# Performance work log

Hardware: AMD Instinct MI355X
Metric: run time of the kernel (lower is better)

## Reference

```python
import jax, jax.numpy as jnp
import numpy as np

B, S, E, H = 2, 2048, 1024, 16
D = E // H  # head_dim = 64
NEG = -1e9


def setup_inputs() -> dict:
    key = jax.random.key(0)
    ks = jax.random.split(key, 12)
    def xavier(k, shape):
        fan_in, fan_out = shape[1], shape[0]
        lim = jnp.sqrt(6.0 / (fan_in + fan_out))
        return jax.random.uniform(k, shape, jnp.float32, -lim, lim)
    inp = {
        'Q_input': jax.random.normal(ks[0], (B, S, E), jnp.float32),
        'K_input': jax.random.normal(ks[1], (B, S, E), jnp.float32),
        'V_input': jax.random.normal(ks[2], (B, S, E), jnp.float32),
        'causal_mask': jnp.where(jnp.tril(jnp.ones((S, S), bool)), 0.0, NEG).astype(jnp.float32),
        'padding_mask': jnp.zeros((B, S), bool),
        'W_q': xavier(ks[3], (E, E)), 'b_q': jnp.zeros((E,), jnp.float32),
        'W_k': xavier(ks[4], (E, E)), 'b_k': jnp.zeros((E,), jnp.float32),
        'W_v': xavier(ks[5], (E, E)), 'b_v': jnp.zeros((E,), jnp.float32),
        'W_o': xavier(ks[6], (E, E)), 'b_o': jnp.zeros((E,), jnp.float32),
    }
    return inp


def reference(Q_input, K_input, V_input, causal_mask, padding_mask,
              W_q, b_q, W_k, b_k, W_v, b_v, W_o, b_o):
    b = Q_input.shape[0]
    # linear proj (torch convention: x @ W.T + b), split into heads -> [B,H,S,D]
    def proj(x, W, bias):
        y = x @ W.T + bias
        return y.reshape(b, -1, H, D).transpose(0, 2, 1, 3)
    Q = proj(Q_input, W_q, b_q)
    K = proj(K_input, W_k, b_k)
    V = proj(V_input, W_v, b_v)
    scale = 1.0 / jnp.sqrt(jnp.float32(D))
    scores = jnp.einsum('bhqd,bhkd->bhqk', Q, K) * scale  # [B,H,Sq,Sk]
    scores = jnp.where(padding_mask[:, None, None, :], NEG, scores)
    scores = scores + causal_mask  # broadcasts [Sq,Sk]
    attn = jax.nn.softmax(scores, axis=-1)
    ctx = jnp.einsum('bhqk,bhkd->bhqd', attn, V)
    ctx = ctx.transpose(0, 2, 1, 3).reshape(b, -1, E)
    return ctx @ W_o.T + b_o
```

## Files before the change

kernel.cpp:

```cpp
#include <hip/hip_runtime.h>
#include <hip/hip_bf16.h>

#define B_ 2
#define S_ 2048
#define E_ 1024
#define H_ 16
#define D_ 64

typedef __bf16 bf16x8 __attribute__((ext_vector_type(8)));
typedef __bf16 bf16x4 __attribute__((ext_vector_type(4)));
typedef float f32x4 __attribute__((ext_vector_type(4)));

#define MFMA16(a, b, c) __builtin_amdgcn_mfma_f32_16x16x32_bf16(a, b, c, 0, 0, 0)

__device__ __forceinline__ void cp16(const void* g, void* l) {
  __builtin_amdgcn_global_load_lds((const __attribute__((address_space(1))) void*)g,
                                   (__attribute__((address_space(3))) void*)l, 16, 0, 0);
}

__global__ __launch_bounds__(256) void cast_all(
    const float* __restrict__ w0, const float* __restrict__ w1,
    const float* __restrict__ w2, const float* __restrict__ w3,
    const float* __restrict__ x0, const float* __restrict__ x1,
    const float* __restrict__ x2,
    __bf16* __restrict__ dW, __bf16* __restrict__ dX)
{
  const int id = blockIdx.x;
  const float* src;
  __bf16* dst;
  size_t i;
  if (id < 2048) {
    const float* ws[4] = {w0, w1, w2, w3};
    int w = id >> 9;
    src = ws[w];
    dst = dW + (size_t)w * E_ * E_;
    i = ((size_t)(id & 511) * 256 + threadIdx.x) * 8;
  } else {
    int e = id - 2048;
    const float* xs[3] = {x0, x1, x2};
    int x = e >> 11;
    src = xs[x];
    dst = dX + (size_t)x * B_ * S_ * E_;
    i = ((size_t)(e & 2047) * 256 + threadIdx.x) * 8;
  }
  f32x4 a = *(const f32x4*)(src + i);
  f32x4 b = *(const f32x4*)(src + i + 4);
  bf16x8 o;
#pragma unroll
  for (int j = 0; j < 4; ++j) { o[j] = (__bf16)a[j]; o[j + 4] = (__bf16)b[j]; }
  *(bf16x8*)(dst + i) = o;
}

__global__ __launch_bounds__(256) void gemm_qkv(
    const __bf16* __restrict__ Xb, const __bf16* __restrict__ Wc,
    const float* __restrict__ bq, const float* __restrict__ bk,
    const float* __restrict__ bv, __bf16* __restrict__ Proj,
    __bf16* __restrict__ Vt)
{
  __shared__ __bf16 As[2][128 * 32];
  __shared__ __bf16 Bs[2][128 * 32];

  const int tid  = threadIdx.x;
  const int wave = tid >> 6, lane = tid & 63;
  const int l15  = lane & 15, quad = lane >> 4;
  const int wr = wave >> 1, wc = wave & 1;
  const int m0 = blockIdx.x * 128;
  const int wid = blockIdx.y >> 3;
  const int n0 = (blockIdx.y & 7) * 128;

  const __bf16* X   = Xb + (size_t)wid * B_ * S_ * E_;
  const float* bias = wid == 0 ? bq : (wid == 1 ? bk : bv);
  const __bf16* W   = Wc + (size_t)wid * E_ * E_;
  __bf16* Out       = Proj + (size_t)wid * B_ * S_ * E_;

  auto stage = [&](int k0, int bi) {
#pragma unroll
    for (int i = 0; i < 2; ++i) {
      int c = i * 256 + tid;
      int row = c >> 2, cg = c & 3;
      cp16(X + (size_t)(m0 + row) * E_ + k0 + cg * 8,
           (char*)&As[bi][0] + i * 4096 + wave * 1024);
    }
#pragma unroll
    for (int i = 0; i < 2; ++i) {
      int c = i * 256 + tid;
      int row = c >> 2, cg = c & 3;
      cp16(W + (size_t)(n0 + row) * E_ + k0 + cg * 8,
           (char*)&Bs[bi][0] + i * 4096 + wave * 1024);
    }
  };

  f32x4 acc[4][4];
#pragma unroll
  for (int i = 0; i < 4; ++i)
#pragma unroll
    for (int j = 0; j < 4; ++j) acc[i][j] = (f32x4){0, 0, 0, 0};

  stage(0, 0);
  int cur = 0;
  for (int k0 = 0; k0 < E_; k0 += 32) {
    if (k0 + 32 < E_) {
      stage(k0 + 32, cur ^ 1);
      asm volatile("s_waitcnt vmcnt(4)" ::: "memory");
    } else {
      asm volatile("s_waitcnt vmcnt(0)" ::: "memory");
    }
    __builtin_amdgcn_s_barrier();

    bf16x8 af[4], bfr[4];
#pragma unroll
    for (int ms = 0; ms < 4; ++ms) {
      int row = wr * 64 + ms * 16 + l15;
      af[ms] = *(const bf16x8*)((const char*)&As[cur][0] + row * 64 + quad * 16);
    }
#pragma unroll
    for (int ns = 0; ns < 4; ++ns) {
      int row = wc * 64 + ns * 16 + l15;
      bfr[ns] = *(const bf16x8*)((const char*)&Bs[cur][0] + row * 64 + quad * 16);
    }
    __builtin_amdgcn_s_setprio(1);
#pragma unroll
    for (int ms = 0; ms < 4; ++ms)
#pragma unroll
      for (int ns = 0; ns < 4; ++ns)
        acc[ms][ns] = MFMA16(af[ms], bfr[ns], acc[ms][ns]);
    __builtin_amdgcn_s_setprio(0);

    asm volatile("" ::: "memory");
    __builtin_amdgcn_s_barrier();
    asm volatile("" ::: "memory");
    cur ^= 1;
  }

  if (wid == 2) {
#pragma unroll
    for (int ns = 0; ns < 4; ++ns) {
      int n = n0 + wc * 64 + ns * 16 + l15;
      float bv_ = bias[n];
      int m_base = m0 + wr * 64 + quad * 4;
      int b = m_base >> 11;
      int s_base = m_base & 2047;
      __bf16* vdst = Vt + (size_t)(b * H_ * D_ + n) * S_ + s_base;
#pragma unroll
      for (int ms = 0; ms < 4; ++ms)
#pragma unroll
        for (int r = 0; r < 4; ++r)
          vdst[ms * 16 + r] = (__bf16)(acc[ms][ns][r] + bv_);
    }
  } else {
    const float osc = (wid == 0) ? 0.18033688011f : 1.0f;
#pragma unroll
    for (int ns = 0; ns < 4; ++ns) {
      int n = n0 + wc * 64 + ns * 16 + l15;
      float bv_ = bias[n];
#pragma unroll
      for (int ms = 0; ms < 4; ++ms)
#pragma unroll
        for (int r = 0; r < 4; ++r) {
          int m = m0 + wr * 64 + ms * 16 + quad * 4 + r;
          Out[(size_t)m * E_ + n] = (__bf16)((acc[ms][ns][r] + bv_) * osc);
        }
    }
  }
}

__global__ __launch_bounds__(256) void gemm_out(
    const __bf16* __restrict__ X, const __bf16* __restrict__ W,
    const float* __restrict__ bias, float* __restrict__ out)
{
  __shared__ __bf16 As[2][64 * 32];
  __shared__ __bf16 Bs[2][128 * 32];

  const int tid  = threadIdx.x;
  const int wave = tid >> 6, lane = tid & 63;
  const int l15  = lane & 15, quad = lane >> 4;
  const int wr = wave >> 1, wc = wave & 1;
  const int m0 = blockIdx.x * 64;
  const int n0 = blockIdx.y * 128;

  auto stage = [&](int k0, int bi) {
    {
      int row = tid >> 2, cg = tid & 3;
      cp16(X + (size_t)(m0 + row) * E_ + k0 + cg * 8,
           (char*)&As[bi][0] + wave * 1024);
    }
#pragma unroll
    for (int i = 0; i < 2; ++i) {
      int c = i * 256 + tid;
      int row = c >> 2, cg = c & 3;
      cp16(W + (size_t)(n0 + row) * E_ + k0 + cg * 8,
           (char*)&Bs[bi][0] + i * 4096 + wave * 1024);
    }
  };

  f32x4 acc[2][4];
#pragma unroll
  for (int i = 0; i < 2; ++i)
#pragma unroll
    for (int j = 0; j < 4; ++j) acc[i][j] = (f32x4){0, 0, 0, 0};

  stage(0, 0);
  int cur = 0;
  for (int k0 = 0; k0 < E_; k0 += 32) {
    if (k0 + 32 < E_) {
      stage(k0 + 32, cur ^ 1);
      asm volatile("s_waitcnt vmcnt(3)" ::: "memory");
    } else {
      asm volatile("s_waitcnt vmcnt(0)" ::: "memory");
    }
    __builtin_amdgcn_s_barrier();

    bf16x8 af[2], bfr[4];
#pragma unroll
    for (int ms = 0; ms < 2; ++ms) {
      int row = wr * 32 + ms * 16 + l15;
      af[ms] = *(const bf16x8*)((const char*)&As[cur][0] + row * 64 + quad * 16);
    }
#pragma unroll
    for (int ns = 0; ns < 4; ++ns) {
      int row = wc * 64 + ns * 16 + l15;
      bfr[ns] = *(const bf16x8*)((const char*)&Bs[cur][0] + row * 64 + quad * 16);
    }
    __builtin_amdgcn_s_setprio(1);
#pragma unroll
    for (int ms = 0; ms < 2; ++ms)
#pragma unroll
      for (int ns = 0; ns < 4; ++ns)
        acc[ms][ns] = MFMA16(af[ms], bfr[ns], acc[ms][ns]);
    __builtin_amdgcn_s_setprio(0);

    asm volatile("" ::: "memory");
    __builtin_amdgcn_s_barrier();
    asm volatile("" ::: "memory");
    cur ^= 1;
  }

#pragma unroll
  for (int ns = 0; ns < 4; ++ns) {
    int n = n0 + wc * 64 + ns * 16 + l15;
    float bv_ = bias[n];
#pragma unroll
    for (int ms = 0; ms < 2; ++ms)
#pragma unroll
      for (int r = 0; r < 4; ++r) {
        int m = m0 + wr * 32 + ms * 16 + quad * 4 + r;
        out[(size_t)m * E_ + n] = acc[ms][ns][r] + bv_;
      }
  }
}

__global__ __launch_bounds__(128, 4) void attn_fwd(
    const __bf16* __restrict__ Qp, const __bf16* __restrict__ Kp,
    const __bf16* __restrict__ Vt, __bf16* __restrict__ Ctx)
{
  const int tid  = threadIdx.x;
  const int wave = tid >> 6;
  const int lane = tid & 63;
  const int l15  = lane & 15;
  const int quad = lane >> 4;
  const int id   = blockIdx.x;
  const int bh   = (id & 7) * 4 + ((id >> 3) & 3);
  const int tile = 63 - (id >> 5);
  const int b    = bh >> 4;
  const int h    = bh & 15;
  const int wq0  = tile * 32 + wave * 16;

  __shared__ __bf16 Ksh[64 * 64];
  __shared__ __bf16 Vsh[64 * 64];

  const __bf16* Khb = Kp + (size_t)b * S_ * E_ + h * 64;
  const __bf16* Vhb = Vt + ((size_t)b * H_ + h) * D_ * S_;

  bf16x8 qa[2];
#pragma unroll
  for (int kk = 0; kk < 2; ++kk)
    qa[kk] = *(const bf16x8*)&Qp[(size_t)(b * S_ + wq0 + l15) * E_ +
                                 h * 64 + kk * 32 + quad * 8];

  f32x4 o[4];
  float rs = 0.f;
#pragma unroll
  for (int ds = 0; ds < 4; ++ds) o[ds] = (f32x4){0, 0, 0, 0};

  const int nch = (tile >> 1) + 1;

  uint4 gk[4], gv[4];
  const int ccr = tid >> 3;
  const int ccg = tid & 7;

  auto issue = [&](int c) {
    const int kb0 = c * 64;
#pragma unroll
    for (int i = 0; i < 4; ++i) {
      int key = i * 16 + ccr;
      const void* ga = Khb + (size_t)(kb0 + key) * E_ + ccg * 8;
      asm volatile("global_load_dwordx4 %0, %1, off"
                   : "=v"(gk[i]) : "v"(ga) : "memory");
    }
#pragma unroll
    for (int i = 0; i < 4; ++i) {
      int d = i * 16 + ccr;
      const void* ga = Vhb + (size_t)d * S_ + kb0 + ccg * 8;
      asm volatile("global_load_dwordx4 %0, %1, off"
                   : "=v"(gv[i]) : "v"(ga) : "memory");
    }
  };
  auto commit = [&]() {
#pragma unroll
    for (int i = 0; i < 4; ++i) {
      int key = i * 16 + ccr;
      *(uint4*)((char*)Ksh + key * 128 + ((ccg ^ (key & 7)) * 16)) = gk[i];
    }
#pragma unroll
    for (int i = 0; i < 4; ++i) {
      int d = i * 16 + ccr;
      *(uint4*)((char*)Vsh + d * 128 + ((ccg ^ (d & 7)) * 16)) = gv[i];
    }
  };

  issue(0);
  asm volatile("s_waitcnt vmcnt(0)" ::: "memory");
  __builtin_amdgcn_sched_barrier(0);
  commit();
  asm volatile("s_waitcnt lgkmcnt(0)" ::: "memory");
  asm volatile("" ::: "memory");
  __builtin_amdgcn_s_barrier();

  for (int c = 0; c < nch; ++c) {
    if (c + 1 < nch) issue(c + 1);
    const int kb0 = c * 64;

    f32x4 sc[4];
    __builtin_amdgcn_s_setprio(1);
#pragma unroll
    for (int ks = 0; ks < 4; ++ks) {
      int row = ks * 16 + l15;
      bf16x8 kf0 = *(const bf16x8*)((const char*)Ksh + row * 128 + (((quad)     ^ (l15 & 7)) * 16));
      bf16x8 kf1 = *(const bf16x8*)((const char*)Ksh + row * 128 + (((4 + quad) ^ (l15 & 7)) * 16));
      f32x4 s = {0, 0, 0, 0};
      s = MFMA16(kf0, qa[0], s);
      s = MFMA16(kf1, qa[1], s);
      sc[ks] = s;
    }
    __builtin_amdgcn_s_setprio(0);

    unsigned pw[4][2];
    const bool msk = (kb0 + 63 > wq0);
    if (msk) {
#pragma unroll
      for (int ks = 0; ks < 4; ++ks) {
        float p[4];
#pragma unroll
        for (int r = 0; r < 4; ++r) {
          float e = exp2f(sc[ks][r]);
          if (kb0 + ks * 16 + quad * 4 + r > wq0 + l15) e = 0.f;
          rs += e;
          p[r] = e;
        }
        asm("v_cvt_pk_bf16_f32 %0, %1, %2" : "=v"(pw[ks][0]) : "v"(p[0]), "v"(p[1]));
        asm("v_cvt_pk_bf16_f32 %0, %1, %2" : "=v"(pw[ks][1]) : "v"(p[2]), "v"(p[3]));
      }
    } else {
#pragma unroll
      for (int ks = 0; ks < 4; ++ks) {
        float p[4];
#pragma unroll
        for (int r = 0; r < 4; ++r) {
          float e = exp2f(sc[ks][r]);
          rs += e;
          p[r] = e;
        }
        asm("v_cvt_pk_bf16_f32 %0, %1, %2" : "=v"(pw[ks][0]) : "v"(p[0]), "v"(p[1]));
        asm("v_cvt_pk_bf16_f32 %0, %1, %2" : "=v"(pw[ks][1]) : "v"(p[2]), "v"(p[3]));
      }
    }

    bf16x8 pf[2];
#pragma unroll
    for (int kk = 0; kk < 2; ++kk) {
      unsigned a0 = pw[2 * kk + 0][0], a1 = pw[2 * kk + 0][1];
      unsigned a2 = pw[2 * kk + 1][0], a3 = pw[2 * kk + 1][1];
      asm("v_permlane32_swap_b32 %0, %1" : "+v"(a0), "+v"(a2));
      asm("v_permlane32_swap_b32 %0, %1" : "+v"(a1), "+v"(a3));
      asm("v_permlane16_swap_b32 %0, %1" : "+v"(a0), "+v"(a2));
      asm("v_permlane16_swap_b32 %0, %1" : "+v"(a1), "+v"(a3));
      union { unsigned u[4]; bf16x8 v; } cvt;
      cvt.u[0] = a0; cvt.u[1] = a1; cvt.u[2] = a2; cvt.u[3] = a3;
      pf[kk] = cvt.v;
    }

    __builtin_amdgcn_s_setprio(1);
#pragma unroll
    for (int ds = 0; ds < 4; ++ds) {
      int row = ds * 16 + l15;
#pragma unroll
      for (int kk = 0; kk < 2; ++kk) {
        bf16x8 vf = *(const bf16x8*)((const char*)Vsh + row * 128 +
                                     (((kk * 4 + quad) ^ (l15 & 7)) * 16));
        o[ds] = MFMA16(pf[kk], vf, o[ds]);
      }
    }
    __builtin_amdgcn_s_setprio(0);

    asm volatile("" ::: "memory");
    __builtin_amdgcn_s_barrier();
    if (c + 1 < nch) {
      asm volatile("s_waitcnt vmcnt(0)" ::: "memory");
      __builtin_amdgcn_sched_barrier(0);
      commit();
      asm volatile("s_waitcnt lgkmcnt(0)" ::: "memory");
    }
    asm volatile("" ::: "memory");
    __builtin_amdgcn_s_barrier();
  }

  float s = rs;
  s += __shfl_xor(s, 16, 64);
  s += __shfl_xor(s, 32, 64);
  float inv = 1.f / s;

#pragma unroll
  for (int r = 0; r < 4; ++r) {
    float invr = __shfl(inv, quad * 4 + r, 64);
    size_t base = (size_t)(b * S_ + wq0 + quad * 4 + r) * E_ + h * 64;
#pragma unroll
    for (int ds = 0; ds < 4; ++ds)
      Ctx[base + ds * 16 + l15] = (__bf16)(o[ds][r] * invr);
  }
}

extern "C" void kernel_launch(void* const* d_in, const int* in_sizes, int n_in,
                              void* d_out, int out_size, void* d_ws, size_t ws_size,
                              hipStream_t stream)
{
  const float* Qin = (const float*)d_in[0];
  const float* Kin = (const float*)d_in[1];
  const float* Vin = (const float*)d_in[2];
  const float* Wq = (const float*)d_in[5];
  const float* bq = (const float*)d_in[6];
  const float* Wk = (const float*)d_in[7];
  const float* bk = (const float*)d_in[8];
  const float* Wv = (const float*)d_in[9];
  const float* bv = (const float*)d_in[10];
  const float* Wo = (const float*)d_in[11];
  const float* bo = (const float*)d_in[12];

  __bf16* ws = (__bf16*)d_ws;
  const size_t WSZ = (size_t)E_ * E_;
  const size_t T   = (size_t)B_ * S_ * E_;
  __bf16* Wc   = ws;
  __bf16* Proj = ws + 4 * WSZ;
  __bf16* Vt   = ws + 4 * WSZ + 3 * T;
  __bf16* Ctx  = ws + 4 * WSZ + 4 * T;
  __bf16* Xbf  = ws + 4 * WSZ + 5 * T;

  cast_all<<<dim3(8192), 256, 0, stream>>>(Wq, Wk, Wv, Wo, Qin, Kin, Vin, Wc, Xbf);
  gemm_qkv<<<dim3(32, 24), 256, 0, stream>>>(Xbf, Wc, bq, bk, bv, Proj, Vt);
  attn_fwd<<<dim3(2048), 128, 0, stream>>>(Proj, Proj + T, Vt, Ctx);
  gemm_out<<<dim3(64, 8), 256, 0, stream>>>(Ctx, Wc + 3 * WSZ, bo, (float*)d_out);
}
```

Baseline: 240.3 us.

## Move V transpose to separate kernel and widen out-projection K tile with swizzle

The QKV GEMM no longer writes V in transposed layout with scattered strided stores. It writes V row-major like Q and K, and a new small kernel transposes it into the layout the attention kernel expects. Separately, the output GEMM doubles its K step to 64 and XOR-swizzles the LDS layout to avoid bank conflicts, which halves the number of barrier iterations. The cost is an extra kernel launch plus an extra read and write pass over V, and more LDS per block in gemm_out.

```diff
diff --git a/kernel.cpp b/kernel.cpp
--- a/kernel.cpp
+++ b/kernel.cpp
@@ -54,8 +54,7 @@
 __global__ __launch_bounds__(256) void gemm_qkv(
     const __bf16* __restrict__ Xb, const __bf16* __restrict__ Wc,
     const float* __restrict__ bq, const float* __restrict__ bk,
-    const float* __restrict__ bv, __bf16* __restrict__ Proj,
-    __bf16* __restrict__ Vt)
+    const float* __restrict__ bv, __bf16* __restrict__ Proj)
 {
   __shared__ __bf16 As[2][128 * 32];
   __shared__ __bf16 Bs[2][128 * 32];
@@ -132,35 +131,18 @@
     cur ^= 1;
   }
 
-  if (wid == 2) {
-#pragma unroll
-    for (int ns = 0; ns < 4; ++ns) {
-      int n = n0 + wc * 64 + ns * 16 + l15;
-      float bv_ = bias[n];
-      int m_base = m0 + wr * 64 + quad * 4;
-      int b = m_base >> 11;
-      int s_base = m_base & 2047;
-      __bf16* vdst = Vt + (size_t)(b * H_ * D_ + n) * S_ + s_base;
-#pragma unroll
-      for (int ms = 0; ms < 4; ++ms)
-#pragma unroll
-        for (int r = 0; r < 4; ++r)
-          vdst[ms * 16 + r] = (__bf16)(acc[ms][ns][r] + bv_);
-    }
-  } else {
-    const float osc = (wid == 0) ? 0.18033688011f : 1.0f;
-#pragma unroll
-    for (int ns = 0; ns < 4; ++ns) {
-      int n = n0 + wc * 64 + ns * 16 + l15;
-      float bv_ = bias[n];
-#pragma unroll
-      for (int ms = 0; ms < 4; ++ms)
-#pragma unroll
-        for (int r = 0; r < 4; ++r) {
-          int m = m0 + wr * 64 + ms * 16 + quad * 4 + r;
-          Out[(size_t)m * E_ + n] = (__bf16)((acc[ms][ns][r] + bv_) * osc);
-        }
-    }
+  const float osc = (wid == 0) ? 0.18033688011f : 1.0f;
+#pragma unroll
+  for (int ns = 0; ns < 4; ++ns) {
+    int n = n0 + wc * 64 + ns * 16 + l15;
+    float bv_ = bias[n];
+#pragma unroll
+    for (int ms = 0; ms < 4; ++ms)
+#pragma unroll
+      for (int r = 0; r < 4; ++r) {
+        int m = m0 + wr * 64 + ms * 16 + quad * 4 + r;
+        Out[(size_t)m * E_ + n] = (__bf16)((acc[ms][ns][r] + bv_) * osc);
+      }
   }
 }
 
@@ -168,8 +150,8 @@
     const __bf16* __restrict__ X, const __bf16* __restrict__ W,
     const float* __restrict__ bias, float* __restrict__ out)
 {
-  __shared__ __bf16 As[2][64 * 32];
-  __shared__ __bf16 Bs[2][128 * 32];
+  __shared__ __bf16 As[2][64 * 64];
+  __shared__ __bf16 Bs[2][128 * 64];
 
   const int tid  = threadIdx.x;
   const int wave = tid >> 6, lane = tid & 63;
@@ -179,16 +161,18 @@
   const int n0 = blockIdx.y * 128;
 
   auto stage = [&](int k0, int bi) {
-    {
-      int row = tid >> 2, cg = tid & 3;
-      cp16(X + (size_t)(m0 + row) * E_ + k0 + cg * 8,
-           (char*)&As[bi][0] + wave * 1024);
-    }
 #pragma unroll
     for (int i = 0; i < 2; ++i) {
       int c = i * 256 + tid;
-      int row = c >> 2, cg = c & 3;
-      cp16(W + (size_t)(n0 + row) * E_ + k0 + cg * 8,
+      int row = c >> 3, cg = c & 7;
+      cp16(X + (size_t)(m0 + row) * E_ + k0 + ((cg ^ (row & 7)) * 8),
+           (char*)&As[bi][0] + i * 4096 + wave * 1024);
+    }
+#pragma unroll
+    for (int i = 0; i < 4; ++i) {
+      int c = i * 256 + tid;
+      int row = c >> 3, cg = c & 7;
+      cp16(W + (size_t)(n0 + row) * E_ + k0 + ((cg ^ (row & 7)) * 8),
            (char*)&Bs[bi][0] + i * 4096 + wave * 1024);
     }
   };
@@ -201,32 +185,40 @@
 
   stage(0, 0);
   int cur = 0;
-  for (int k0 = 0; k0 < E_; k0 += 32) {
-    if (k0 + 32 < E_) {
-      stage(k0 + 32, cur ^ 1);
-      asm volatile("s_waitcnt vmcnt(3)" ::: "memory");
+  for (int k0 = 0; k0 < E_; k0 += 64) {
+    if (k0 + 64 < E_) {
+      stage(k0 + 64, cur ^ 1);
+      asm volatile("s_waitcnt vmcnt(6)" ::: "memory");
     } else {
       asm volatile("s_waitcnt vmcnt(0)" ::: "memory");
     }
     __builtin_amdgcn_s_barrier();
 
-    bf16x8 af[2], bfr[4];
+    bf16x8 af[2][2], bfr[4][2];
 #pragma unroll
     for (int ms = 0; ms < 2; ++ms) {
       int row = wr * 32 + ms * 16 + l15;
-      af[ms] = *(const bf16x8*)((const char*)&As[cur][0] + row * 64 + quad * 16);
+#pragma unroll
+      for (int kk = 0; kk < 2; ++kk)
+        af[ms][kk] = *(const bf16x8*)((const char*)&As[cur][0] + row * 128 +
+                                      (((kk * 4 + quad) ^ (row & 7)) * 16));
     }
 #pragma unroll
     for (int ns = 0; ns < 4; ++ns) {
       int row = wc * 64 + ns * 16 + l15;
-      bfr[ns] = *(const bf16x8*)((const char*)&Bs[cur][0] + row * 64 + quad * 16);
+#pragma unroll
+      for (int kk = 0; kk < 2; ++kk)
+        bfr[ns][kk] = *(const bf16x8*)((const char*)&Bs[cur][0] + row * 128 +
+                                       (((kk * 4 + quad) ^ (row & 7)) * 16));
     }
     __builtin_amdgcn_s_setprio(1);
 #pragma unroll
     for (int ms = 0; ms < 2; ++ms)
 #pragma unroll
       for (int ns = 0; ns < 4; ++ns)
-        acc[ms][ns] = MFMA16(af[ms], bfr[ns], acc[ms][ns]);
+#pragma unroll
+        for (int kk = 0; kk < 2; ++kk)
+          acc[ms][ns] = MFMA16(af[ms][kk], bfr[ns][kk], acc[ms][ns]);
     __builtin_amdgcn_s_setprio(0);
 
     asm volatile("" ::: "memory");
@@ -246,6 +238,28 @@
         int m = m0 + wr * 32 + ms * 16 + quad * 4 + r;
         out[(size_t)m * E_ + n] = acc[ms][ns][r] + bv_;
       }
+  }
+}
+
+__global__ __launch_bounds__(64) void transpose_v(
+    const __bf16* __restrict__ Vp, __bf16* __restrict__ Vt)
+{
+  const int lane = threadIdx.x;
+  const int b = blockIdx.y >> 4;
+  const int h = blockIdx.y & 15;
+  const int s0 = blockIdx.x * 64 + (lane & 7) * 8;
+  const int d0 = (lane >> 3) * 8;
+
+  bf16x8 in[8];
+#pragma unroll
+  for (int j = 0; j < 8; ++j)
+    in[j] = *(const bf16x8*)&Vp[(((size_t)b * S_ + s0 + j) * H_ + h) * D_ + d0];
+#pragma unroll
+  for (int i = 0; i < 8; ++i) {
+    bf16x8 t;
+#pragma unroll
+    for (int j = 0; j < 8; ++j) t[j] = in[j][i];
+    *(bf16x8*)&Vt[(((size_t)b * H_ + h) * D_ + d0 + i) * S_ + s0] = t;
   }
 }
 
@@ -455,7 +469,8 @@
   __bf16* Xbf  = ws + 4 * WSZ + 5 * T;
 
   cast_all<<<dim3(8192), 256, 0, stream>>>(Wq, Wk, Wv, Wo, Qin, Kin, Vin, Wc, Xbf);
-  gemm_qkv<<<dim3(32, 24), 256, 0, stream>>>(Xbf, Wc, bq, bk, bv, Proj, Vt);
+  gemm_qkv<<<dim3(32, 24), 256, 0, stream>>>(Xbf, Wc, bq, bk, bv, Proj);
+  transpose_v<<<dim3(S_ / 64, B_ * H_), 64, 0, stream>>>(Proj + 2 * T, Vt);
   attn_fwd<<<dim3(2048), 128, 0, stream>>>(Proj, Proj + T, Vt, Ctx);
   gemm_out<<<dim3(64, 8), 256, 0, stream>>>(Ctx, Wc + 3 * WSZ, bo, (float*)d_out);
 }
```

Measured after the change: 228.7 us. 1.05x faster.
